# Optimization experiments

Measured on AMD Instinct MI355X. Metric: run time of the kernel, lower is better.

The kernel has to match this reference:

```python
import jax, jax.numpy as jnp
import numpy as np

B, L, H, E, R = 2, 512, 768, 512, 32768
H2 = H // 2


def setup_inputs() -> dict:
    key = jax.random.key(0)
    ks = jax.random.split(key, 16)
    s = 0.02
    inp = {
        "hidden_states": jax.random.normal(ks[0], (B, L, H), dtype=jnp.float32),
        "ent_start": jax.random.randint(ks[1], (B, E), 0, L, dtype=jnp.int32),
        "ent_label": jax.random.randint(ks[2], (B, E), 0, 3, dtype=jnp.int32),
        "rel_head": jax.random.randint(ks[3], (B, R), 0, E, dtype=jnp.int32),
        "rel_tail": jax.random.randint(ks[4], (B, R), 0, E, dtype=jnp.int32),
        "rel_label": jax.random.randint(ks[5], (B, R), 0, 2, dtype=jnp.int32),
        "entity_emb": jax.random.normal(ks[6], (3, H), dtype=jnp.float32) * s,
        "head_W1": jax.random.normal(ks[7], (2 * H, H), dtype=jnp.float32) * s,
        "head_b1": jnp.zeros((H,), dtype=jnp.float32),
        "head_W2": jax.random.normal(ks[8], (H, H2), dtype=jnp.float32) * s,
        "head_b2": jnp.zeros((H2,), dtype=jnp.float32),
        "tail_W1": jax.random.normal(ks[9], (2 * H, H), dtype=jnp.float32) * s,
        "tail_b1": jnp.zeros((H,), dtype=jnp.float32),
        "tail_W2": jax.random.normal(ks[10], (H, H2), dtype=jnp.float32) * s,
        "tail_b2": jnp.zeros((H2,), dtype=jnp.float32),
        "bil_W": jax.random.normal(ks[11], (2, H2, H2), dtype=jnp.float32) * s,
        "lin_W": jax.random.normal(ks[12], (2 * H2, 2), dtype=jnp.float32) * s,
        "lin_b": jnp.zeros((2,), dtype=jnp.float32),
    }
    return inp


def _mlp(x, W1, b1, W2, b2):
    # Linear -> ReLU -> (dropout=identity) -> Linear -> ReLU -> (dropout=identity)
    h = jax.nn.relu(jnp.einsum("brd,dh->brh", x, W1) + b1)
    return jax.nn.relu(jnp.einsum("brh,hk->brk", h, W2) + b2)


def reference(hidden_states, ent_start, ent_label, rel_head, rel_tail, rel_label,
              entity_emb, head_W1, head_b1, head_W2, head_b2,
              tail_W1, tail_b1, tail_W2, tail_b2, bil_W, lin_W, lin_b):
    # Gather entity start token index and label for each relation endpoint
    h_idx = jnp.take_along_axis(ent_start, rel_head, axis=1)  # [B,R]
    t_idx = jnp.take_along_axis(ent_start, rel_tail, axis=1)
    h_lab = jnp.take_along_axis(ent_label, rel_head, axis=1)
    t_lab = jnp.take_along_axis(ent_label, rel_tail, axis=1)

    # Gather hidden states at entity start positions: [B,R,H]
    h_tok = jnp.take_along_axis(hidden_states, h_idx[..., None], axis=1)
    t_tok = jnp.take_along_axis(hidden_states, t_idx[..., None], axis=1)

    head_repr = jnp.concatenate([h_tok, entity_emb[h_lab]], axis=-1)  # [B,R,2H]
    tail_repr = jnp.concatenate([t_tok, entity_emb[t_lab]], axis=-1)

    heads = _mlp(head_repr, head_W1, head_b1, head_W2, head_b2)  # [B,R,H2]
    tails = _mlp(tail_repr, tail_W1, tail_b1, tail_W2, tail_b2)

    # BiaffineAttention: bilinear(x1,x2) + linear(cat(x1,x2))
    bil = jnp.einsum("brd,ode,bre->bro", heads, bil_W, tails)  # [B,R,2]
    lin = jnp.einsum("brc,co->bro", jnp.concatenate([heads, tails], axis=-1), lin_W) + lin_b
    logits = bil + lin  # [B,R,2]

    # Per-doc mean cross-entropy, summed over docs (matches loss accumulation)
    logp = jax.nn.log_softmax(logits, axis=-1)
    ce = -jnp.take_along_axis(logp, rel_label[..., None], axis=-1)[..., 0]  # [B,R]
    loss = ce.mean(axis=-1).sum()

    return loss, logits.reshape(B * R, 2)
```

## Files before the change

kernel.cpp:

```cpp
#include <hip/hip_runtime.h>
#include <math.h>

#define BB 2
#define LL 512
#define HH 768
#define EE 512
#define RR 32768
#define H2 384
#define MM 1024

typedef __attribute__((ext_vector_type(8))) short     bf16x8;
typedef __attribute__((ext_vector_type(4))) float     f32x4;
typedef __attribute__((ext_vector_type(8))) unsigned short u16x8;

__device__ __forceinline__ unsigned short f2bf(float f) {
    unsigned int u = __float_as_uint(f);
    u = (u + 0x7FFFu + ((u >> 16) & 1u)) >> 16;
    return (unsigned short)u;
}

__global__ __launch_bounds__(256) void prep(
    const float* __restrict__ hW1, const float* __restrict__ tW1,
    const float* __restrict__ hW2, const float* __restrict__ tW2,
    const float* __restrict__ bilW,
    unsigned short* __restrict__ W1ht, unsigned short* __restrict__ W1tt,
    unsigned short* __restrict__ W2ht, unsigned short* __restrict__ W2tt,
    unsigned short* __restrict__ bW0t, unsigned short* __restrict__ bW1t,
    const float* __restrict__ hidden, const int* __restrict__ ent_start,
    const int* __restrict__ ent_label, const float* __restrict__ emb,
    const float* __restrict__ hb1, const float* __restrict__ tb1,
    unsigned short* __restrict__ Hbf, float* __restrict__ embc)
{
    __shared__ unsigned short T[32 * 40];
    __shared__ float red[4][192];
    const int bid = blockIdx.x;
    const int t = threadIdx.x;

    if (bid >= 3040) {
        const int eb = bid - 3040;
        const int tc = t & 63;
        const int kg = t >> 6;
        const int n = eb * 64 + tc;
        const float* W = (n < 768) ? hW1 : tW1;
        const int cc = (n < 768) ? n : n - 768;
        float a0 = 0.f, a1 = 0.f, a2 = 0.f;
        const int kbeg = kg * 192;
        #pragma unroll 8
        for (int k = kbeg; k < kbeg + 192; ++k) {
            const float w = W[(size_t)(768 + k) * 768 + cc];
            a0 += emb[k] * w;
            a1 += emb[768 + k] * w;
            a2 += emb[1536 + k] * w;
        }
        red[kg][0 * 64 + tc] = a0;
        red[kg][1 * 64 + tc] = a1;
        red[kg][2 * 64 + tc] = a2;
        __syncthreads();
        if (kg == 0) {
            const float b = (n < 768) ? hb1[n] : tb1[n - 768];
            #pragma unroll
            for (int l = 0; l < 3; ++l) {
                embc[l * 1536 + n] = b + red[0][l * 64 + tc] + red[1][l * 64 + tc]
                                       + red[2][l * 64 + tc] + red[3][l * 64 + tc];
            }
        }
        return;
    }

    if (bid >= 2016) {
        const int m = bid - 2016;
        if (t >= 96) return;
        const int b = m >> 9;
        const int idx = ent_start[m];
        const float4* s = (const float4*)(hidden + (size_t)(b * LL + idx) * HH);
        const float4 v0 = s[2 * t];
        const float4 v1 = s[2 * t + 1];
        u16x8 o;
        o[0] = f2bf(v0.x); o[1] = f2bf(v0.y); o[2] = f2bf(v0.z); o[3] = f2bf(v0.w);
        o[4] = f2bf(v1.x); o[5] = f2bf(v1.y); o[6] = f2bf(v1.z); o[7] = f2bf(v1.w);
        *(u16x8*)(Hbf + (size_t)m * 768 + 8 * t) = o;
        return;
    }

    const float* src; unsigned short* dst; int K, N, tile;
    if (bid < 576)       { src = hW1;            dst = W1ht; K = 768; N = 768; tile = bid; }
    else if (bid < 1152) { src = tW1;            dst = W1tt; K = 768; N = 768; tile = bid - 576; }
    else if (bid < 1440) { src = hW2;            dst = W2ht; K = 768; N = 384; tile = bid - 1152; }
    else if (bid < 1728) { src = tW2;            dst = W2tt; K = 768; N = 384; tile = bid - 1440; }
    else if (bid < 1872) { src = bilW;           dst = bW0t; K = 384; N = 384; tile = bid - 1728; }
    else                 { src = bilW + 384*384; dst = bW1t; K = 384; N = 384; tile = bid - 1872; }
    const int tn = N >> 5;
    const int n0 = (tile % tn) * 32;
    const int k0 = (tile / tn) * 32;

    const int r  = t >> 3;
    const int c4 = (t & 7) * 4;
    const float4 g = *(const float4*)(src + (size_t)(k0 + r) * N + n0 + c4);
    T[(c4 + 0) * 40 + r] = f2bf(g.x);
    T[(c4 + 1) * 40 + r] = f2bf(g.y);
    T[(c4 + 2) * 40 + r] = f2bf(g.z);
    T[(c4 + 3) * 40 + r] = f2bf(g.w);
    __syncthreads();
    const int n  = t >> 3;
    const int k4 = (t & 7) * 4;
    *(ushort4*)(dst + (size_t)(n0 + n) * K + k0 + k4) = *(ushort4*)&T[n * 40 + k4];
}

template<bool RELU, bool BIAS, bool EB, bool WF32, bool WBF16, bool O2>
__global__ __launch_bounds__(256) void gemm_mfma(
    const unsigned short* __restrict__ A, int lda, int aoff1,
    const unsigned short* __restrict__ Bt0, const unsigned short* __restrict__ Bt1,
    int ldb, int bt_mrow, int Nh,
    const float* __restrict__ bias0, const float* __restrict__ bias1,
    const float* __restrict__ embc, const int* __restrict__ labels,
    int K, float* __restrict__ Cf, unsigned short* __restrict__ Cb, int ldc)
{
    __shared__ unsigned short As[64 * 40];
    __shared__ unsigned short Bs[64 * 40];

    const int tid = threadIdx.x;
    const int n0 = blockIdx.x * 64;
    const int m0 = blockIdx.y * 64;
    const int hf = (n0 >= Nh) ? 1 : 0;
    const unsigned short* Bt = hf ? Bt1 : Bt0;
    const int nc0 = n0 - (hf ? Nh : 0);
    const int aoff = hf ? aoff1 : 0;

    const int sr = tid >> 2;
    const int sk = (tid & 3) * 8;

    const unsigned short* Ap = A + (size_t)(m0 + sr) * lda + aoff + sk;
    const unsigned short* Bp = Bt + (size_t)((m0 >> 9) * bt_mrow + nc0 + sr) * ldb + sk;

    const int lane = tid & 63;
    const int wave = tid >> 6;
    const int wm = (wave & 1) * 32;
    const int wn = (wave >> 1) * 32;
    const int l15 = lane & 15;
    const int quad = lane >> 4;

    f32x4 acc00 = {}, acc01 = {}, acc10 = {}, acc11 = {};

    u16x8 av = *(const u16x8*)(Ap);
    u16x8 bv = *(const u16x8*)(Bp);

    for (int k0 = 0; k0 < K; k0 += 32) {
        __syncthreads();
        *(u16x8*)&As[sr * 40 + sk] = av;
        *(u16x8*)&Bs[sr * 40 + sk] = bv;
        __syncthreads();
        if (k0 + 32 < K) {
            av = *(const u16x8*)(Ap + k0 + 32);
            bv = *(const u16x8*)(Bp + k0 + 32);
        }
        const bf16x8 a0 = *(const bf16x8*)&As[(wm + l15) * 40 + quad * 8];
        const bf16x8 a1 = *(const bf16x8*)&As[(wm + 16 + l15) * 40 + quad * 8];
        const bf16x8 b0 = *(const bf16x8*)&Bs[(wn + l15) * 40 + quad * 8];
        const bf16x8 b1 = *(const bf16x8*)&Bs[(wn + 16 + l15) * 40 + quad * 8];
        acc00 = __builtin_amdgcn_mfma_f32_16x16x32_bf16(a0, b0, acc00, 0, 0, 0);
        acc01 = __builtin_amdgcn_mfma_f32_16x16x32_bf16(a0, b1, acc01, 0, 0, 0);
        acc10 = __builtin_amdgcn_mfma_f32_16x16x32_bf16(a1, b0, acc10, 0, 0, 0);
        acc11 = __builtin_amdgcn_mfma_f32_16x16x32_bf16(a1, b1, acc11, 0, 0, 0);
    }

    float bias_v0 = 0.f, bias_v1 = 0.f;
    if (BIAS) {
        const float* bb = hf ? bias1 : bias0;
        bias_v0 = bb[nc0 + wn + l15];
        bias_v1 = bb[nc0 + wn + 16 + l15];
    }
    const f32x4 accs[2][2] = {{acc00, acc01}, {acc10, acc11}};
    #pragma unroll
    for (int mi = 0; mi < 2; ++mi) {
        int labr[4];
        if (EB) {
            #pragma unroll
            for (int r = 0; r < 4; ++r)
                labr[r] = labels[m0 + wm + mi * 16 + quad * 4 + r];
        }
        #pragma unroll
        for (int ni = 0; ni < 2; ++ni) {
            const int col = n0 + wn + ni * 16 + l15;
            const float bv = ni ? bias_v1 : bias_v0;
            int colw = col;
            if (O2) colw = 2 * (nc0 + wn + ni * 16 + l15) + hf;
            #pragma unroll
            for (int r = 0; r < 4; ++r) {
                const int row = m0 + wm + mi * 16 + quad * 4 + r;
                float v = accs[mi][ni][r];
                if (BIAS) v += bv;
                if (EB) v += embc[labr[r] * 1536 + col];
                if (RELU) v = fmaxf(v, 0.f);
                if (WF32) Cf[(size_t)row * ldc + colw] = v;
                if (WBF16) Cb[(size_t)row * ldc + colw] = f2bf(v);
            }
        }
    }
}

__global__ __launch_bounds__(256) void lin_proj(
    const float* __restrict__ HT, const float* __restrict__ linW,
    float* __restrict__ hlin, float* __restrict__ tlin)
{
    const int tid = threadIdx.x;
    const int lane = tid & 63;
    const int wave = tid >> 6;
    const int m = blockIdx.x * 4 + wave;
    const float* hr = HT + (size_t)m * 768;
    const float* tr = hr + 384;
    float hl0 = 0.f, hl1 = 0.f, tl0 = 0.f, tl1 = 0.f;
    #pragma unroll
    for (int t = 0; t < 6; ++t) {
        const int c = lane + 64 * t;
        const float hv = hr[c];
        const float tv = tr[c];
        const float2 wh = *(const float2*)(linW + 2 * c);
        const float2 wt = *(const float2*)(linW + 2 * (384 + c));
        hl0 += hv * wh.x; hl1 += hv * wh.y;
        tl0 += tv * wt.x; tl1 += tv * wt.y;
    }
    #pragma unroll
    for (int o = 32; o >= 1; o >>= 1) {
        hl0 += __shfl_xor(hl0, o, 64);
        hl1 += __shfl_xor(hl1, o, 64);
        tl0 += __shfl_xor(tl0, o, 64);
        tl1 += __shfl_xor(tl1, o, 64);
    }
    if (lane == 0) {
        hlin[2 * m]     = hl0;
        hlin[2 * m + 1] = hl1;
        tlin[2 * m]     = tl0;
        tlin[2 * m + 1] = tl1;
    }
}

__global__ __launch_bounds__(256) void rel_gather(
    const float* __restrict__ Stab,
    const float* __restrict__ hlin, const float* __restrict__ tlin,
    const float* __restrict__ lin_b,
    const int* __restrict__ rel_head, const int* __restrict__ rel_tail,
    const int* __restrict__ rel_label,
    float* __restrict__ out, float* __restrict__ bsum)
{
    const int tid = threadIdx.x;
    const int i = blockIdx.x * 256 + tid;
    const int b = i >> 15;
    const int h = rel_head[i];
    const int t = rel_tail[i];
    const int lab = rel_label[i];
    const int mh = (b << 9) + h;
    const int mt = (b << 9) + t;

    const float2 hl = ((const float2*)hlin)[mh];
    const float2 tl = ((const float2*)tlin)[mt];
    const float2 zz = *(const float2*)(Stab + (size_t)mh * 1024 + 2 * t);
    const float z0 = zz.x + hl.x + tl.x + lin_b[0];
    const float z1 = zz.y + hl.y + tl.y + lin_b[1];
    out[1 + 2 * (size_t)i]     = z0;
    out[2 + 2 * (size_t)i]     = z1;

    const float mx = fmaxf(z0, z1);
    const float mn = fminf(z0, z1);
    const float lse = mx + log1pf(expf(mn - mx));
    float ce = lse - (lab ? z1 : z0);

    #pragma unroll
    for (int o = 32; o >= 1; o >>= 1) ce += __shfl_xor(ce, o, 64);
    __shared__ float wsum[4];
    if ((tid & 63) == 0) wsum[tid >> 6] = ce;
    __syncthreads();
    if (tid == 0) bsum[blockIdx.x] = wsum[0] + wsum[1] + wsum[2] + wsum[3];
}

__global__ __launch_bounds__(256) void finalize(
    const float* __restrict__ bsum, float* __restrict__ out)
{
    const int tid = threadIdx.x;
    float v = bsum[tid];
    #pragma unroll
    for (int o = 32; o >= 1; o >>= 1) v += __shfl_xor(v, o, 64);
    __shared__ float s[4];
    if ((tid & 63) == 0) s[tid >> 6] = v;
    __syncthreads();
    if (tid == 0) {
        out[0] = (s[0] + s[1] + s[2] + s[3]) * (1.0f / (float)RR);
    }
}

extern "C" void kernel_launch(void* const* d_in, const int* in_sizes, int n_in,
                              void* d_out, int out_size, void* d_ws, size_t ws_size,
                              hipStream_t stream) {
    const float* hidden    = (const float*)d_in[0];
    const int*   ent_start = (const int*)d_in[1];
    const int*   ent_label = (const int*)d_in[2];
    const int*   rel_head  = (const int*)d_in[3];
    const int*   rel_tail  = (const int*)d_in[4];
    const int*   rel_label = (const int*)d_in[5];
    const float* emb       = (const float*)d_in[6];
    const float* head_W1   = (const float*)d_in[7];
    const float* head_b1   = (const float*)d_in[8];
    const float* head_W2   = (const float*)d_in[9];
    const float* head_b2   = (const float*)d_in[10];
    const float* tail_W1   = (const float*)d_in[11];
    const float* tail_b1   = (const float*)d_in[12];
    const float* tail_W2   = (const float*)d_in[13];
    const float* tail_b2   = (const float*)d_in[14];
    const float* bil_W     = (const float*)d_in[15];
    const float* lin_W     = (const float*)d_in[16];
    const float* lin_b     = (const float*)d_in[17];
    float* out = (float*)d_out;

    char* w = (char*)d_ws;
    auto carve = [&](size_t bytes) {
        char* p = w; w += (bytes + 255) & ~(size_t)255; return p;
    };
    unsigned short* Hbf  = (unsigned short*)carve((size_t)MM * 768 * 2);
    unsigned short* Y1bf = (unsigned short*)carve((size_t)MM * 1536 * 2);
    unsigned short* HTbf = (unsigned short*)carve((size_t)MM * 768 * 2);
    float*          HT   = (float*)carve((size_t)MM * 768 * 4);
    unsigned short* hWbf = (unsigned short*)carve((size_t)MM * 768 * 2);
    float*          Stab = (float*)carve((size_t)MM * 1024 * 4);
    unsigned short* W1ht = (unsigned short*)carve((size_t)768 * 768 * 2);
    unsigned short* W1tt = (unsigned short*)carve((size_t)768 * 768 * 2);
    unsigned short* W2ht = (unsigned short*)carve((size_t)384 * 768 * 2);
    unsigned short* W2tt = (unsigned short*)carve((size_t)384 * 768 * 2);
    unsigned short* bW0t = (unsigned short*)carve((size_t)384 * 384 * 2);
    unsigned short* bW1t = (unsigned short*)carve((size_t)384 * 384 * 2);
    float*          embc = (float*)carve((size_t)3 * 1536 * 4);
    float*          hlin = (float*)carve(2048 * 4);
    float*          tlin = (float*)carve(2048 * 4);
    float*          bsum = (float*)carve(256 * 4);

    prep<<<3064, 256, 0, stream>>>(
        head_W1, tail_W1, head_W2, tail_W2, bil_W,
        W1ht, W1tt, W2ht, W2tt, bW0t, bW1t,
        hidden, ent_start, ent_label, emb, head_b1, tail_b1, Hbf, embc);

    gemm_mfma<true, false, true, false, true, false><<<dim3(24, 16), 256, 0, stream>>>(
        Hbf, 768, 0, W1ht, W1tt, 768, 0, 768, nullptr, nullptr, embc, ent_label,
        768, nullptr, Y1bf, 1536);

    gemm_mfma<true, true, false, true, true, false><<<dim3(12, 16), 256, 0, stream>>>(
        Y1bf, 1536, 768, W2ht, W2tt, 768, 0, 384, head_b2, tail_b2, nullptr, nullptr,
        768, HT, HTbf, 768);

    gemm_mfma<false, false, false, false, true, false><<<dim3(12, 16), 256, 0, stream>>>(
        HTbf, 768, 0, bW0t, bW1t, 384, 0, 384, nullptr, nullptr, nullptr, nullptr,
        384, nullptr, hWbf, 768);

    gemm_mfma<false, false, false, true, false, true><<<dim3(16, 16), 256, 0, stream>>>(
        hWbf, 768, 384, HTbf + 384, HTbf + 384, 768, 512, 512,
        nullptr, nullptr, nullptr, nullptr, 384, Stab, nullptr, 1024);

    lin_proj<<<256, 256, 0, stream>>>(HT, lin_W, hlin, tlin);

    rel_gather<<<256, 256, 0, stream>>>(Stab, hlin, tlin, lin_b,
                                        rel_head, rel_tail, rel_label, out, bsum);

    finalize<<<1, 256, 0, stream>>>(bsum, out);
}
```

Baseline: 149.5 us.

## Double-buffer GEMM k-tiles, fuse linear projection into GEMM epilogue, drop finalize kernel

The MFMA GEMM now stages 64-wide k-tiles in double-buffered shared memory with a single barrier per iteration, so global loads for the next tile overlap with the current MFMAs. The lin_proj kernel and the fp32 HT buffer are removed: the second GEMM's epilogue computes the linear-head dot products with shuffles and accumulates them into hlin/tlin with atomics. The finalize kernel is removed: the loss is accumulated with atomicAdd, and an extra prep block zeroes the accumulators first. This cuts two launches and some memory traffic, at the cost of more shared memory, atomic contention and non-deterministic float summation order.

```diff
diff --git a/kernel.cpp b/kernel.cpp
--- a/kernel.cpp
+++ b/kernel.cpp
@@ -29,12 +29,21 @@
     const float* __restrict__ hidden, const int* __restrict__ ent_start,
     const int* __restrict__ ent_label, const float* __restrict__ emb,
     const float* __restrict__ hb1, const float* __restrict__ tb1,
-    unsigned short* __restrict__ Hbf, float* __restrict__ embc)
+    unsigned short* __restrict__ Hbf, float* __restrict__ embc,
+    float* __restrict__ hlin, float* __restrict__ tlin, float* __restrict__ out)
 {
     __shared__ unsigned short T[32 * 40];
     __shared__ float red[4][192];
     const int bid = blockIdx.x;
     const int t = threadIdx.x;
+
+    if (bid == 3064) {
+        const float4 z = {0.f, 0.f, 0.f, 0.f};
+        ((float4*)hlin)[t] = z; ((float4*)hlin)[256 + t] = z;
+        ((float4*)tlin)[t] = z; ((float4*)tlin)[256 + t] = z;
+        if (t == 0) out[0] = 0.f;
+        return;
+    }
 
     if (bid >= 3040) {
         const int eb = bid - 3040;
@@ -106,17 +115,18 @@
     *(ushort4*)(dst + (size_t)(n0 + n) * K + k0 + k4) = *(ushort4*)&T[n * 40 + k4];
 }
 
-template<bool RELU, bool BIAS, bool EB, bool WF32, bool WBF16, bool O2>
+template<bool RELU, bool BIAS, bool EB, bool WF32, bool WBF16, bool O2, bool LIN>
 __global__ __launch_bounds__(256) void gemm_mfma(
     const unsigned short* __restrict__ A, int lda, int aoff1,
     const unsigned short* __restrict__ Bt0, const unsigned short* __restrict__ Bt1,
     int ldb, int bt_mrow, int Nh,
     const float* __restrict__ bias0, const float* __restrict__ bias1,
     const float* __restrict__ embc, const int* __restrict__ labels,
+    const float* __restrict__ linW, float* __restrict__ hlin, float* __restrict__ tlin,
     int K, float* __restrict__ Cf, unsigned short* __restrict__ Cb, int ldc)
 {
-    __shared__ unsigned short As[64 * 40];
-    __shared__ unsigned short Bs[64 * 40];
+    __shared__ unsigned short As[2][64 * 72];
+    __shared__ unsigned short Bs[2][64 * 72];
 
     const int tid = threadIdx.x;
     const int n0 = blockIdx.x * 64;
@@ -127,7 +137,7 @@
     const int aoff = hf ? aoff1 : 0;
 
     const int sr = tid >> 2;
-    const int sk = (tid & 3) * 8;
+    const int sk = (tid & 3) * 16;
 
     const unsigned short* Ap = A + (size_t)(m0 + sr) * lda + aoff + sk;
     const unsigned short* Bp = Bt + (size_t)((m0 >> 9) * bt_mrow + nc0 + sr) * ldb + sk;
@@ -141,26 +151,51 @@
 
     f32x4 acc00 = {}, acc01 = {}, acc10 = {}, acc11 = {};
 
-    u16x8 av = *(const u16x8*)(Ap);
-    u16x8 bv = *(const u16x8*)(Bp);
-
-    for (int k0 = 0; k0 < K; k0 += 32) {
-        __syncthreads();
-        *(u16x8*)&As[sr * 40 + sk] = av;
-        *(u16x8*)&Bs[sr * 40 + sk] = bv;
-        __syncthreads();
-        if (k0 + 32 < K) {
-            av = *(const u16x8*)(Ap + k0 + 32);
-            bv = *(const u16x8*)(Bp + k0 + 32);
-        }
-        const bf16x8 a0 = *(const bf16x8*)&As[(wm + l15) * 40 + quad * 8];
-        const bf16x8 a1 = *(const bf16x8*)&As[(wm + 16 + l15) * 40 + quad * 8];
-        const bf16x8 b0 = *(const bf16x8*)&Bs[(wn + l15) * 40 + quad * 8];
-        const bf16x8 b1 = *(const bf16x8*)&Bs[(wn + 16 + l15) * 40 + quad * 8];
-        acc00 = __builtin_amdgcn_mfma_f32_16x16x32_bf16(a0, b0, acc00, 0, 0, 0);
-        acc01 = __builtin_amdgcn_mfma_f32_16x16x32_bf16(a0, b1, acc01, 0, 0, 0);
-        acc10 = __builtin_amdgcn_mfma_f32_16x16x32_bf16(a1, b0, acc10, 0, 0, 0);
-        acc11 = __builtin_amdgcn_mfma_f32_16x16x32_bf16(a1, b1, acc11, 0, 0, 0);
+    u16x8 a0v = *(const u16x8*)(Ap);
+    u16x8 a1v = *(const u16x8*)(Ap + 8);
+    u16x8 b0v = *(const u16x8*)(Bp);
+    u16x8 b1v = *(const u16x8*)(Bp + 8);
+    const int swo = sr * 72 + sk;
+    *(u16x8*)&As[0][swo] = a0v; *(u16x8*)&As[0][swo + 8] = a1v;
+    *(u16x8*)&Bs[0][swo] = b0v; *(u16x8*)&Bs[0][swo + 8] = b1v;
+
+    const int NT = K >> 6;
+    const int aro = quad * 8;
+    int cur = 0;
+    for (int it = 0; it < NT; ++it) {
+        if (it + 1 < NT) {
+            const int ko = (it + 1) * 64;
+            a0v = *(const u16x8*)(Ap + ko); a1v = *(const u16x8*)(Ap + ko + 8);
+            b0v = *(const u16x8*)(Bp + ko); b1v = *(const u16x8*)(Bp + ko + 8);
+        }
+        asm volatile("s_waitcnt lgkmcnt(0)" ::: "memory");
+        __builtin_amdgcn_s_barrier();
+        __builtin_amdgcn_sched_barrier(0);
+        const unsigned short* Ac = As[cur];
+        const unsigned short* Bc = Bs[cur];
+        const bf16x8 fa0 = *(const bf16x8*)&Ac[(wm + l15) * 72 + aro];
+        const bf16x8 fa1 = *(const bf16x8*)&Ac[(wm + 16 + l15) * 72 + aro];
+        const bf16x8 fb0 = *(const bf16x8*)&Bc[(wn + l15) * 72 + aro];
+        const bf16x8 fb1 = *(const bf16x8*)&Bc[(wn + 16 + l15) * 72 + aro];
+        const bf16x8 ga0 = *(const bf16x8*)&Ac[(wm + l15) * 72 + aro + 32];
+        const bf16x8 ga1 = *(const bf16x8*)&Ac[(wm + 16 + l15) * 72 + aro + 32];
+        const bf16x8 gb0 = *(const bf16x8*)&Bc[(wn + l15) * 72 + aro + 32];
+        const bf16x8 gb1 = *(const bf16x8*)&Bc[(wn + 16 + l15) * 72 + aro + 32];
+        acc00 = __builtin_amdgcn_mfma_f32_16x16x32_bf16(fa0, fb0, acc00, 0, 0, 0);
+        acc01 = __builtin_amdgcn_mfma_f32_16x16x32_bf16(fa0, fb1, acc01, 0, 0, 0);
+        acc10 = __builtin_amdgcn_mfma_f32_16x16x32_bf16(fa1, fb0, acc10, 0, 0, 0);
+        acc11 = __builtin_amdgcn_mfma_f32_16x16x32_bf16(fa1, fb1, acc11, 0, 0, 0);
+        acc00 = __builtin_amdgcn_mfma_f32_16x16x32_bf16(ga0, gb0, acc00, 0, 0, 0);
+        acc01 = __builtin_amdgcn_mfma_f32_16x16x32_bf16(ga0, gb1, acc01, 0, 0, 0);
+        acc10 = __builtin_amdgcn_mfma_f32_16x16x32_bf16(ga1, gb0, acc10, 0, 0, 0);
+        acc11 = __builtin_amdgcn_mfma_f32_16x16x32_bf16(ga1, gb1, acc11, 0, 0, 0);
+        if (it + 1 < NT) {
+            unsigned short* Aw = &As[cur ^ 1][0];
+            unsigned short* Bw = &Bs[cur ^ 1][0];
+            *(u16x8*)&Aw[swo] = a0v; *(u16x8*)&Aw[swo + 8] = a1v;
+            *(u16x8*)&Bw[swo] = b0v; *(u16x8*)&Bw[swo + 8] = b1v;
+        }
+        cur ^= 1;
     }
 
     float bias_v0 = 0.f, bias_v1 = 0.f;
@@ -169,68 +204,57 @@
         bias_v0 = bb[nc0 + wn + l15];
         bias_v1 = bb[nc0 + wn + 16 + l15];
     }
+    const int col0 = n0 + wn + l15;
+    const int col1 = col0 + 16;
+    int colw0 = col0, colw1 = col1;
+    if (O2) {
+        colw0 = 2 * (nc0 + wn + l15) + hf;
+        colw1 = 2 * (nc0 + wn + 16 + l15) + hf;
+    }
+    float2 lw0 = {0.f, 0.f}, lw1 = {0.f, 0.f};
+    float* lout = nullptr;
+    if (LIN) {
+        lw0 = ((const float2*)linW)[col0];
+        lw1 = ((const float2*)linW)[col1];
+        lout = hf ? tlin : hlin;
+    }
     const f32x4 accs[2][2] = {{acc00, acc01}, {acc10, acc11}};
     #pragma unroll
     for (int mi = 0; mi < 2; ++mi) {
-        int labr[4];
-        if (EB) {
-            #pragma unroll
-            for (int r = 0; r < 4; ++r)
-                labr[r] = labels[m0 + wm + mi * 16 + quad * 4 + r];
-        }
         #pragma unroll
-        for (int ni = 0; ni < 2; ++ni) {
-            const int col = n0 + wn + ni * 16 + l15;
-            const float bv = ni ? bias_v1 : bias_v0;
-            int colw = col;
-            if (O2) colw = 2 * (nc0 + wn + ni * 16 + l15) + hf;
-            #pragma unroll
-            for (int r = 0; r < 4; ++r) {
-                const int row = m0 + wm + mi * 16 + quad * 4 + r;
-                float v = accs[mi][ni][r];
-                if (BIAS) v += bv;
-                if (EB) v += embc[labr[r] * 1536 + col];
-                if (RELU) v = fmaxf(v, 0.f);
-                if (WF32) Cf[(size_t)row * ldc + colw] = v;
-                if (WBF16) Cb[(size_t)row * ldc + colw] = f2bf(v);
-            }
-        }
-    }
-}
-
-__global__ __launch_bounds__(256) void lin_proj(
-    const float* __restrict__ HT, const float* __restrict__ linW,
-    float* __restrict__ hlin, float* __restrict__ tlin)
-{
-    const int tid = threadIdx.x;
-    const int lane = tid & 63;
-    const int wave = tid >> 6;
-    const int m = blockIdx.x * 4 + wave;
-    const float* hr = HT + (size_t)m * 768;
-    const float* tr = hr + 384;
-    float hl0 = 0.f, hl1 = 0.f, tl0 = 0.f, tl1 = 0.f;
-    #pragma unroll
-    for (int t = 0; t < 6; ++t) {
-        const int c = lane + 64 * t;
-        const float hv = hr[c];
-        const float tv = tr[c];
-        const float2 wh = *(const float2*)(linW + 2 * c);
-        const float2 wt = *(const float2*)(linW + 2 * (384 + c));
-        hl0 += hv * wh.x; hl1 += hv * wh.y;
-        tl0 += tv * wt.x; tl1 += tv * wt.y;
-    }
-    #pragma unroll
-    for (int o = 32; o >= 1; o >>= 1) {
-        hl0 += __shfl_xor(hl0, o, 64);
-        hl1 += __shfl_xor(hl1, o, 64);
-        tl0 += __shfl_xor(tl0, o, 64);
-        tl1 += __shfl_xor(tl1, o, 64);
-    }
-    if (lane == 0) {
-        hlin[2 * m]     = hl0;
-        hlin[2 * m + 1] = hl1;
-        tlin[2 * m]     = tl0;
-        tlin[2 * m + 1] = tl1;
+        for (int r = 0; r < 4; ++r) {
+            const int row = m0 + wm + mi * 16 + quad * 4 + r;
+            float v0 = accs[mi][0][r];
+            float v1 = accs[mi][1][r];
+            if (BIAS) { v0 += bias_v0; v1 += bias_v1; }
+            if (EB) {
+                const int lab = labels[row];
+                v0 += embc[lab * 1536 + col0];
+                v1 += embc[lab * 1536 + col1];
+            }
+            if (RELU) { v0 = fmaxf(v0, 0.f); v1 = fmaxf(v1, 0.f); }
+            if (WF32) {
+                Cf[(size_t)row * ldc + colw0] = v0;
+                Cf[(size_t)row * ldc + colw1] = v1;
+            }
+            if (WBF16) {
+                Cb[(size_t)row * ldc + colw0] = f2bf(v0);
+                Cb[(size_t)row * ldc + colw1] = f2bf(v1);
+            }
+            if (LIN) {
+                float s0 = v0 * lw0.x + v1 * lw1.x;
+                float s1 = v0 * lw0.y + v1 * lw1.y;
+                #pragma unroll
+                for (int o = 8; o >= 1; o >>= 1) {
+                    s0 += __shfl_xor(s0, o, 64);
+                    s1 += __shfl_xor(s1, o, 64);
+                }
+                if (l15 == 0) {
+                    atomicAdd(&lout[2 * row],     s0);
+                    atomicAdd(&lout[2 * row + 1], s1);
+                }
+            }
+        }
     }
 }
 
@@ -240,7 +264,7 @@
     const float* __restrict__ lin_b,
     const int* __restrict__ rel_head, const int* __restrict__ rel_tail,
     const int* __restrict__ rel_label,
-    float* __restrict__ out, float* __restrict__ bsum)
+    float* __restrict__ out)
 {
     const int tid = threadIdx.x;
     const int i = blockIdx.x * 256 + tid;
@@ -269,21 +293,9 @@
     __shared__ float wsum[4];
     if ((tid & 63) == 0) wsum[tid >> 6] = ce;
     __syncthreads();
-    if (tid == 0) bsum[blockIdx.x] = wsum[0] + wsum[1] + wsum[2] + wsum[3];
-}
-
-__global__ __launch_bounds__(256) void finalize(
-    const float* __restrict__ bsum, float* __restrict__ out)
-{
-    const int tid = threadIdx.x;
-    float v = bsum[tid];
-    #pragma unroll
-    for (int o = 32; o >= 1; o >>= 1) v += __shfl_xor(v, o, 64);
-    __shared__ float s[4];
-    if ((tid & 63) == 0) s[tid >> 6] = v;
-    __syncthreads();
     if (tid == 0) {
-        out[0] = (s[0] + s[1] + s[2] + s[3]) * (1.0f / (float)RR);
+        const float bs = wsum[0] + wsum[1] + wsum[2] + wsum[3];
+        atomicAdd(out, bs * (1.0f / (float)RR));
     }
 }
 
@@ -317,7 +329,6 @@
     unsigned short* Hbf  = (unsigned short*)carve((size_t)MM * 768 * 2);
     unsigned short* Y1bf = (unsigned short*)carve((size_t)MM * 1536 * 2);
     unsigned short* HTbf = (unsigned short*)carve((size_t)MM * 768 * 2);
-    float*          HT   = (float*)carve((size_t)MM * 768 * 4);
     unsigned short* hWbf = (unsigned short*)carve((size_t)MM * 768 * 2);
     float*          Stab = (float*)carve((size_t)MM * 1024 * 4);
     unsigned short* W1ht = (unsigned short*)carve((size_t)768 * 768 * 2);
@@ -329,33 +340,34 @@
     float*          embc = (float*)carve((size_t)3 * 1536 * 4);
     float*          hlin = (float*)carve(2048 * 4);
     float*          tlin = (float*)carve(2048 * 4);
-    float*          bsum = (float*)carve(256 * 4);
-
-    prep<<<3064, 256, 0, stream>>>(
+
+    prep<<<3065, 256, 0, stream>>>(
         head_W1, tail_W1, head_W2, tail_W2, bil_W,
         W1ht, W1tt, W2ht, W2tt, bW0t, bW1t,
-        hidden, ent_start, ent_label, emb, head_b1, tail_b1, Hbf, embc);
-
-    gemm_mfma<true, false, true, false, true, false><<<dim3(24, 16), 256, 0, stream>>>(
+        hidden, ent_start, ent_label, emb, head_b1, tail_b1, Hbf, embc,
+        hlin, tlin, out);
+
+    gemm_mfma<true, false, true, false, true, false, false>
+        <<<dim3(24, 16), 256, 0, stream>>>(
         Hbf, 768, 0, W1ht, W1tt, 768, 0, 768, nullptr, nullptr, embc, ent_label,
-        768, nullptr, Y1bf, 1536);
-
-    gemm_mfma<true, true, false, true, true, false><<<dim3(12, 16), 256, 0, stream>>>(
+        nullptr, nullptr, nullptr, 768, nullptr, Y1bf, 1536);
+
+    gemm_mfma<true, true, false, false, true, false, true>
+        <<<dim3(12, 16), 256, 0, stream>>>(
         Y1bf, 1536, 768, W2ht, W2tt, 768, 0, 384, head_b2, tail_b2, nullptr, nullptr,
-        768, HT, HTbf, 768);
-
-    gemm_mfma<false, false, false, false, true, false><<<dim3(12, 16), 256, 0, stream>>>(
+        lin_W, hlin, tlin, 768, nullptr, HTbf, 768);
+
+    gemm_mfma<false, false, false, false, true, false, false>
+        <<<dim3(12, 16), 256, 0, stream>>>(
         HTbf, 768, 0, bW0t, bW1t, 384, 0, 384, nullptr, nullptr, nullptr, nullptr,
-        384, nullptr, hWbf, 768);
-
-    gemm_mfma<false, false, false, true, false, true><<<dim3(16, 16), 256, 0, stream>>>(
+        nullptr, nullptr, nullptr, 384, nullptr, hWbf, 768);
+
+    gemm_mfma<false, false, false, true, false, true, false>
+        <<<dim3(16, 16), 256, 0, stream>>>(
         hWbf, 768, 384, HTbf + 384, HTbf + 384, 768, 512, 512,
-        nullptr, nullptr, nullptr, nullptr, 384, Stab, nullptr, 1024);
-
-    lin_proj<<<256, 256, 0, stream>>>(HT, lin_W, hlin, tlin);
+        nullptr, nullptr, nullptr, nullptr,
+        nullptr, nullptr, nullptr, 384, Stab, nullptr, 1024);
 
     rel_gather<<<256, 256, 0, stream>>>(Stab, hlin, tlin, lin_b,
-                                        rel_head, rel_tail, rel_label, out, bsum);
-
-    finalize<<<1, 256, 0, stream>>>(bsum, out);
-}
+                                        rel_head, rel_tail, rel_label, out);
+}
```

Result: faster. 142.5 us (-4.7%).
